# Kernel optimization log

Measured on AMD Instinct MI355X. Metric: run time of the kernel, lower is better.

Reference implementation:

```python
import jax, jax.numpy as jnp
import numpy as np

HEADS = 8

def _rotate_every_two(t):
    # t: [..., d]; interleaved rotation (-x2, x1) pairs
    x1 = t[..., ::2]
    x2 = t[..., 1::2]
    return jnp.stack([-x2, x1], axis=-1).reshape(t.shape)

def _theta_shift(t, sin, cos):
    return t * cos + _rotate_every_two(t) * sin

def setup_inputs() -> dict:
    key = jax.random.key(0)
    ks = jax.random.split(key, 5)
    B, H, W, C = 4, 40, 40, 512
    dh = C // HEADS
    x = jax.random.normal(ks[0], (B, H, W, C), dtype=jnp.float32)
    sin = jax.random.normal(ks[1], (H, W, dh), dtype=jnp.float32)
    cos = jax.random.normal(ks[2], (H, W, dh), dtype=jnp.float32)
    # 1x1 conv weight [3C, C] (kernel dims squeezed) + bias
    w_qkv = jax.random.normal(ks[3], (3 * C, C), dtype=jnp.float32) * (C ** -0.5)
    b_qkv = jnp.zeros((3 * C,), dtype=jnp.float32)
    return {"x": x, "sin": sin, "cos": cos, "w_qkv": w_qkv, "b_qkv": b_qkv}

def reference(x, sin, cos, w_qkv, b_qkv):
    B, H, W, C = x.shape
    heads = HEADS
    dh = C // heads
    scale = dh ** -0.5
    # 1x1 conv == per-pixel linear projection
    qkv = jnp.einsum('bhwc,oc->bhwo', x, w_qkv) + b_qkv  # [B,H,W,3C]
    q, k, v = jnp.split(qkv, 3, axis=-1)

    def to_heads(t):
        # channel order is (heads, dim_head) per the torch rearrange
        return t.reshape(B, H, W, heads, dh).transpose(0, 3, 1, 2, 4)  # [B,heads,H,W,dh]

    q = _theta_shift(to_heads(q), sin, cos)
    k = _theta_shift(to_heads(k), sin, cos)
    # v is computed but unused downstream in the original module (bug preserved)

    N = H * W
    q = q.reshape(B, heads, N, dh)
    k = k.reshape(B, heads, N, dh)

    attn = jnp.einsum('bhnd,bhmd->bhnm', q, k) * scale  # [B,heads,N,N]
    p = jax.nn.softmax(attn, axis=-1)
    # NOTE: original code does matmul(logist, kfine_heads) — K, not V. Kept faithful.
    out = jnp.einsum('bhnm,bhmd->bhnd', p, k)  # [B,heads,N,dh]
    out = out.transpose(0, 2, 1, 3).reshape(B, H, W, C)
    return out
```

## Files before the change

### kernel.cpp

```cpp
#include <hip/hip_runtime.h>
#include <hip/hip_bf16.h>


typedef __hip_bfloat16 bf16;
typedef __attribute__((ext_vector_type(8))) short short8;
typedef __attribute__((ext_vector_type(4))) short bfx4;
typedef __attribute__((ext_vector_type(4))) float f32x4;

#define NSP 1600
#define CDIM 512
#define DH 64

__device__ __forceinline__ f32x4 mfma32(short8 a, short8 b, f32x4 c) {
  return __builtin_amdgcn_mfma_f32_16x16x32_bf16(a, b, c, 0, 0, 0);
}

#if __has_builtin(__builtin_amdgcn_mfma_f32_16x16x16bf16_1k)
__device__ __forceinline__ f32x4 mfma_k16(bfx4 a, bfx4 b, f32x4 c) {
  return __builtin_amdgcn_mfma_f32_16x16x16bf16_1k(a, b, c, 0, 0, 0);
}
#else
__device__ __forceinline__ f32x4 mfma_k16(bfx4 a, bfx4 b, f32x4 c) {
  short8 a8 = {a.x, a.y, a.z, a.w, 0, 0, 0, 0};
  short8 b8 = {b.x, b.y, b.z, b.w, 0, 0, 0, 0};
  return __builtin_amdgcn_mfma_f32_16x16x32_bf16(a8, b8, c, 0, 0, 0);
}
#endif

__device__ __forceinline__ short8 cvt8(float4 v0, float4 v1) {
  short8 r; bf16* p = (bf16*)&r;
  p[0] = __float2bfloat16(v0.x); p[1] = __float2bfloat16(v0.y);
  p[2] = __float2bfloat16(v0.z); p[3] = __float2bfloat16(v0.w);
  p[4] = __float2bfloat16(v1.x); p[5] = __float2bfloat16(v1.y);
  p[6] = __float2bfloat16(v1.z); p[7] = __float2bfloat16(v1.w);
  return r;
}

extern "C" __global__ __launch_bounds__(256)
void cvt_kernel(const float* __restrict__ x, const float* __restrict__ w,
                const float* __restrict__ sin_t, const float* __restrict__ cos_t,
                bf16* __restrict__ x_bf, bf16* __restrict__ w_bf,
                float* __restrict__ sinT, float* __restrict__ cosT)
{
  __shared__ float t_lds[64][68];
  const int bid = blockIdx.x, tid = threadIdx.x;
  if (bid < 1600) {
    const size_t i = (size_t)bid * 2048 + tid * 8;
    float4 v0 = *(const float4*)(x + i);
    float4 v1 = *(const float4*)(x + i + 4);
    *(short8*)(x_bf + i) = cvt8(v0, v1);
  } else if (bid < 1856) {
    const size_t i = (size_t)(bid - 1600) * 2048 + tid * 8;
    float4 v0 = *(const float4*)(w + i);
    float4 v1 = *(const float4*)(w + i + 4);
    *(short8*)(w_bf + i) = cvt8(v0, v1);
  } else {
    const int t = bid - 1856;
    const float* src = (t < 25) ? sin_t : cos_t;
    float* dst = (t < 25) ? sinT : cosT;
    const int nt = (t < 25) ? t : t - 25;
    const int r = tid >> 2, c = (tid & 3) * 16;
#pragma unroll
    for (int j = 0; j < 4; ++j)
      *(float4*)&t_lds[r][c + j * 4] =
          *(const float4*)(src + (size_t)(nt * 64 + r) * 64 + c + j * 4);
    __syncthreads();
#pragma unroll
    for (int j4 = 0; j4 < 4; ++j4) {
      float4 o;
      o.x = t_lds[c + j4 * 4 + 0][r];
      o.y = t_lds[c + j4 * 4 + 1][r];
      o.z = t_lds[c + j4 * 4 + 2][r];
      o.w = t_lds[c + j4 * 4 + 3][r];
      *(float4*)(dst + (size_t)r * NSP + nt * 64 + c + j4 * 4) = o;
    }
  }
}

extern "C" __global__ __launch_bounds__(256)
void proj_kernel(const bf16* __restrict__ x_bf, const bf16* __restrict__ w_bf,
                 const float* __restrict__ bias, const float* __restrict__ sinT,
                 const float* __restrict__ cosT, bf16* __restrict__ q_ws,
                 bf16* __restrict__ k2_ws, bf16* __restrict__ kt2_ws)
{
  __shared__ __align__(16) char smem[27648];
  bf16 (*x_lds)[72] = (bf16(*)[72])smem;
  bf16 (*w_lds)[72] = (bf16(*)[72])(smem + 18432);
  bf16* ep = (bf16*)smem;

  const int tid  = threadIdx.x;
  const int wave = tid >> 6;
  const int lane = tid & 63;
  const int col  = lane & 15;
  const int quad = lane >> 4;
  const int wm = wave >> 1, wo = wave & 1;
  const int m0 = blockIdx.x * 128;
  const int o0 = blockIdx.y * 64;

  f32x4 acc[4][2];
#pragma unroll
  for (int i = 0; i < 4; ++i)
#pragma unroll
    for (int j = 0; j < 2; ++j) acc[i][j] = {0.f, 0.f, 0.f, 0.f};

  const int srow = tid >> 1;
  const int sch  = (tid & 1) * 32;
  const int wrow = tid >> 2;
  const int wch  = (tid & 3) * 16;

  for (int kt = 0; kt < 8; ++kt) {
    __syncthreads();
    {
      const bf16* xs = x_bf + (size_t)(m0 + srow) * CDIM + kt * 64 + sch;
#pragma unroll
      for (int j = 0; j < 4; ++j)
        *(short8*)&x_lds[srow][sch + j * 8] = *(const short8*)(xs + j * 8);
      const bf16* ws = w_bf + (size_t)(o0 + wrow) * CDIM + kt * 64 + wch;
#pragma unroll
      for (int j = 0; j < 2; ++j)
        *(short8*)&w_lds[wrow][wch + j * 8] = *(const short8*)(ws + j * 8);
    }
    __syncthreads();
#pragma unroll
    for (int half = 0; half < 2; ++half) {
      short8 af[4], bfr[2];
#pragma unroll
      for (int mt = 0; mt < 4; ++mt)
        af[mt] = *(short8*)&x_lds[wm * 64 + mt * 16 + col][half * 32 + quad * 8];
#pragma unroll
      for (int ot = 0; ot < 2; ++ot)
        bfr[ot] = *(short8*)&w_lds[wo * 32 + ot * 16 + col][half * 32 + quad * 8];
#pragma unroll
      for (int mt = 0; mt < 4; ++mt)
#pragma unroll
        for (int ot = 0; ot < 2; ++ot)
          acc[mt][ot] = mfma32(af[mt], bfr[ot], acc[mt][ot]);
    }
  }

  __syncthreads();
  const int b_idx = (m0 + wm * 64) / NSP;
  const int n0w   = m0 + wm * 64 - b_idx * NSP;
  const bool isq  = (o0 < 512);
#pragma unroll
  for (int ot = 0; ot < 2; ++ot) {
    const int o_local = wo * 32 + ot * 16 + col;
    const int o_g = o0 + o_local;
    const float bv = bias[o_g];
    const int d = o_g & 63;
#pragma unroll
    for (int mt = 0; mt < 4; ++mt) {
      const int nl = mt * 16 + quad * 4;
      float t[4], rot[4];
#pragma unroll
      for (int r = 0; r < 4; ++r) t[r] = acc[mt][ot][r] + bv;
#pragma unroll
      for (int r = 0; r < 4; ++r) {
        float tp = __shfl_xor(t[r], 1, 64);
        rot[r] = (lane & 1) ? tp : -tp;
      }
      const float4 c4 = *(const float4*)(cosT + (size_t)d * NSP + n0w + nl);
      const float4 s4 = *(const float4*)(sinT + (size_t)d * NSP + n0w + nl);
      float res[4];
      res[0] = t[0] * c4.x + rot[0] * s4.x;
      res[1] = t[1] * c4.y + rot[1] * s4.y;
      res[2] = t[2] * c4.z + rot[2] * s4.z;
      res[3] = t[3] * c4.w + rot[3] * s4.w;
      if (isq) {
#pragma unroll
        for (int r = 0; r < 4; ++r) res[r] *= 0.125f;
      }
      bfx4 pk; bf16* pp = (bf16*)&pk;
#pragma unroll
      for (int r = 0; r < 4; ++r) pp[r] = __float2bfloat16(res[r]);
      *(bfx4*)&ep[o_local * 132 + wm * 64 + nl] = pk;
    }
  }
  __syncthreads();

  if (isq) {
    const int m_l = tid >> 1, hf = tid & 1;
    const int gm = m0 + m_l;
    const int bi = gm / NSP, n = gm - bi * NSP;
    const int h = o0 >> 6;
    bf16* base = q_ws + ((size_t)(bi * 8 + h) * NSP + n) * 64 + hf * 32;
#pragma unroll
    for (int c = 0; c < 4; ++c) {
      short8 v; bf16* vp = (bf16*)&v;
#pragma unroll
      for (int j = 0; j < 8; ++j) vp[j] = ep[(hf * 32 + c * 8 + j) * 132 + m_l];
      *(short8*)(base + c * 8) = v;
    }
  } else {
    const int h = (o0 - 512) >> 6;
#pragma unroll
    for (int it = 0; it < 4; ++it) {
      const int ci = it * 256 + tid;
      const int T = (ci >> 9) & 1, inner = ci & 511;
      const int ccol = inner & 15, cq = (inner >> 4) & 3;
      const int f = (inner >> 6) & 1, ti = (inner >> 7) & 1, kh2 = (inner >> 8) & 1;
      const int gmb = m0 + T * 64;
      const int bi = gmb / NSP, ktile = (gmb - bi * NSP) >> 6;
      const int m_l = T * 64 + (2 * kh2 + ti) * 16 + ccol;
      const int er0 = (f * 4 + cq) * 8;
      short8 v; bf16* vp = (bf16*)&v;
#pragma unroll
      for (int j = 0; j < 8; ++j) vp[j] = ep[(er0 + j) * 132 + m_l];
      *(short8*)(k2_ws +
          (((size_t)(bi * 8 + h) * 25 + ktile) * 512 + inner) * 8) = v;
    }
#pragma unroll
    for (int it = 0; it < 4; ++it) {
      const int ci = it * 256 + tid;
      const int T = (ci >> 9) & 1, inner = ci & 511;
      const int ccol = inner & 15, cq = (inner >> 4) & 3;
      const int dt = (inner >> 6) & 3, kh2 = (inner >> 8) & 1;
      const int gmb = m0 + T * 64;
      const int bi = gmb / NSP, ktile = (gmb - bi * NSP) >> 6;
      const bf16* eprow =
          ep + (dt * 16 + ccol) * 132 + T * 64 + kh2 * 32 + cq * 4;
      short8 v;
      ((bfx4*)&v)[0] = *(const bfx4*)(eprow);
      ((bfx4*)&v)[1] = *(const bfx4*)(eprow + 16);
      *(short8*)(kt2_ws +
          (((size_t)(bi * 8 + h) * 25 + ktile) * 512 + inner) * 8) = v;
    }
  }
}


#define LOADF(KF, KTF, KT)                                                    \
  {                                                                           \
    const bf16* kc_  = k2b  + (KT) * 4096;                                    \
    const bf16* kc2_ = kt2b + (KT) * 4096;                                    \
    _Pragma("unroll")                                                         \
    for (int ti = 0; ti < 2; ++ti)                                            \
      _Pragma("unroll")                                                       \
      for (int f = 0; f < 2; ++f)                                             \
        KF[ti][f] =                                                           \
            *(const short8*)(kc_ + (((kh * 2 + ti) * 2 + f) * 64 + lane) * 8);\
    _Pragma("unroll")                                                         \
    for (int dt = 0; dt < 4; ++dt)                                            \
      KTF[dt] = *(const short8*)(kc2_ + ((kh * 4 + dt) * 64 + lane) * 8);     \
  }

#define COMPUTEF(KF, KTF)                                                     \
  {                                                                           \
    f32x4 s[2][2];                                                            \
    _Pragma("unroll")                                                         \
    for (int ti = 0; ti < 2; ++ti)                                            \
      _Pragma("unroll")                                                       \
      for (int ct = 0; ct < 2; ++ct) {                                        \
        f32x4 t = {0.f, 0.f, 0.f, 0.f};                                       \
        t = mfma32(KF[ti][0], qb[ct][0], t);                                  \
        t = mfma32(KF[ti][1], qb[ct][1], t);                                  \
        s[ti][ct] = t;                                                        \
      }                                                                       \
    bfx4 p4[2][2];                                                            \
    _Pragma("unroll")                                                         \
    for (int ti = 0; ti < 2; ++ti)                                            \
      _Pragma("unroll")                                                       \
      for (int ct = 0; ct < 2; ++ct) {                                        \
        _Pragma("unroll")                                                     \
        for (int r = 0; r < 4; ++r) s[ti][ct][r] = __expf(s[ti][ct][r]);      \
        l_part[ct] +=                                                         \
            s[ti][ct][0] + s[ti][ct][1] + s[ti][ct][2] + s[ti][ct][3];        \
        bf16* pp = (bf16*)&p4[ti][ct];                                        \
        _Pragma("unroll")                                                     \
        for (int r = 0; r < 4; ++r) pp[r] = __float2bfloat16(s[ti][ct][r]);   \
      }                                                                       \
    _Pragma("unroll")                                                         \
    for (int dt = 0; dt < 4; ++dt) {                                          \
      bfx4 alo = __builtin_shufflevector(KTF[dt], KTF[dt], 0, 1, 2, 3);       \
      bfx4 ahi = __builtin_shufflevector(KTF[dt], KTF[dt], 4, 5, 6, 7);       \
      _Pragma("unroll")                                                       \
      for (int ct = 0; ct < 2; ++ct) {                                        \
        oacc[dt][ct] = mfma_k16(alo, p4[0][ct], oacc[dt][ct]);                \
        oacc[dt][ct] = mfma_k16(ahi, p4[1][ct], oacc[dt][ct]);                \
      }                                                                       \
    }                                                                         \
  }

extern "C" __global__ __launch_bounds__(256, 2)
void attn_kernel(const bf16* __restrict__ q_ws, const bf16* __restrict__ k2_ws,
                 const bf16* __restrict__ kt2_ws, float* __restrict__ out)
{
  __shared__ float red[2][64][36];

  const int id = blockIdx.x;
  const int xr = id & 7, inner = id >> 3;
  const int qt = inner % 25;
  const int bh = (inner / 25) * 8 + xr;
  const int b = bh >> 3, h = bh & 7;
  const int tid  = threadIdx.x;
  const int wave = tid >> 6;
  const int lane = tid & 63;
  const int col  = lane & 15;
  const int quad = lane >> 4;
  const int qg = wave & 1, kh = wave >> 1;

  short8 qb[2][2];
#pragma unroll
  for (int ct = 0; ct < 2; ++ct) {
    const bf16* qp =
        q_ws + ((size_t)bh * NSP + qt * 64 + (qg * 2 + ct) * 16 + col) * 64;
    qb[ct][0] = *(const short8*)(qp + quad * 8);
    qb[ct][1] = *(const short8*)(qp + 32 + quad * 8);
  }

  f32x4 oacc[4][2];
#pragma unroll
  for (int i = 0; i < 4; ++i)
#pragma unroll
    for (int j = 0; j < 2; ++j) oacc[i][j] = {0.f, 0.f, 0.f, 0.f};
  float l_part[2] = {0.f, 0.f};

  const bf16* k2b  = k2_ws  + (size_t)bh * 25 * 4096;
  const bf16* kt2b = kt2_ws + (size_t)bh * 25 * 4096;

  short8 kfA[2][2], ktfA[4], kfB[2][2], ktfB[4];
  LOADF(kfA, ktfA, 0)
#pragma unroll 1
  for (int i = 0; i < 12; ++i) {
    LOADF(kfB, ktfB, 2 * i + 1)
    COMPUTEF(kfA, ktfA)
    LOADF(kfA, ktfA, 2 * i + 2)
    COMPUTEF(kfB, ktfB)
  }
  COMPUTEF(kfA, ktfA)

#pragma unroll
  for (int ct = 0; ct < 2; ++ct) {
    l_part[ct] += __shfl_xor(l_part[ct], 16, 64);
    l_part[ct] += __shfl_xor(l_part[ct], 32, 64);
  }

  if (wave >= 2) {
    float* dst = &red[wave - 2][lane][0];
#pragma unroll
    for (int dt = 0; dt < 4; ++dt)
#pragma unroll
      for (int ct = 0; ct < 2; ++ct)
        *(f32x4*)(dst + (dt * 2 + ct) * 4) = oacc[dt][ct];
    dst[32] = l_part[0]; dst[33] = l_part[1];
  }
  __syncthreads();
  if (wave < 2) {
    const float* srcr = &red[wave][lane][0];
#pragma unroll
    for (int dt = 0; dt < 4; ++dt)
#pragma unroll
      for (int ct = 0; ct < 2; ++ct)
        oacc[dt][ct] += *(const f32x4*)(srcr + (dt * 2 + ct) * 4);
    const float inv0 = 1.f / (l_part[0] + srcr[32]);
    const float inv1 = 1.f / (l_part[1] + srcr[33]);
#pragma unroll
    for (int ct = 0; ct < 2; ++ct) {
      const float inv = ct ? inv1 : inv0;
      const int qrow = qt * 64 + (qg * 2 + ct) * 16 + col;
      float* ob = out + ((size_t)b * NSP + qrow) * CDIM + h * 64;
#pragma unroll
      for (int dt = 0; dt < 4; ++dt) {
        float4 v;
        v.x = oacc[dt][ct][0] * inv; v.y = oacc[dt][ct][1] * inv;
        v.z = oacc[dt][ct][2] * inv; v.w = oacc[dt][ct][3] * inv;
        *(float4*)(ob + dt * 16 + quad * 4) = v;
      }
    }
  }
}

extern "C" void kernel_launch(void* const* d_in, const int* in_sizes, int n_in,
                              void* d_out, int out_size, void* d_ws, size_t ws_size,
                              hipStream_t stream) {
  const float* x     = (const float*)d_in[0];
  const float* sin_t = (const float*)d_in[1];
  const float* cos_t = (const float*)d_in[2];
  const float* w_qkv = (const float*)d_in[3];
  const float* b_qkv = (const float*)d_in[4];
  float* out = (float*)d_out;

  const size_t QK = (size_t)32 * NSP * DH;
  bf16* q_ws   = (bf16*)d_ws;
  bf16* k2_ws  = q_ws + QK;
  bf16* kt2_ws = k2_ws + QK;
  bf16* x_bf   = kt2_ws + QK;
  bf16* w_bf   = x_bf + (size_t)6400 * CDIM;
  float* sinT  = (float*)(w_bf + (size_t)1024 * CDIM);
  float* cosT  = sinT + (size_t)DH * NSP;

  cvt_kernel<<<1906, 256, 0, stream>>>(x, w_qkv, sin_t, cos_t, x_bf, w_bf, sinT, cosT);

  dim3 gproj(50, 16);
  proj_kernel<<<gproj, 256, 0, stream>>>(x_bf, w_bf, b_qkv, sinT, cosT,
                                         q_ws, k2_ws, kt2_ws);

  attn_kernel<<<800, 256, 0, stream>>>(q_ws, k2_ws, kt2_ws, out);
}
```

Measured before the change: 137.0 us.

## Split attention key tiles across eight waves per block with two-stage reduction

Doubles the attention block from 4 to 8 waves. Each wave now handles one 16-key subtile instead of two, so per-wave MFMA work, register fragments and the KT loads (now 4-element halves) are halved. The partial outputs and softmax denominators are combined with an extra LDS reduction stage and barrier. This aims to raise latency hiding and occupancy on the key loop, at the cost of more shared memory, more reduction traffic and an extra synchronization.

```diff
diff --git a/kernel.cpp b/kernel.cpp
--- a/kernel.cpp
+++ b/kernel.cpp
@@ -233,59 +233,46 @@
   {                                                                           \
     const bf16* kc_  = k2b  + (KT) * 4096;                                    \
     const bf16* kc2_ = kt2b + (KT) * 4096;                                    \
-    _Pragma("unroll")                                                         \
-    for (int ti = 0; ti < 2; ++ti)                                            \
-      _Pragma("unroll")                                                       \
-      for (int f = 0; f < 2; ++f)                                             \
-        KF[ti][f] =                                                           \
-            *(const short8*)(kc_ + (((kh * 2 + ti) * 2 + f) * 64 + lane) * 8);\
+    KF[0] = *(const short8*)(kc_ + ((kh * 2 + 0) * 64 + lane) * 8);           \
+    KF[1] = *(const short8*)(kc_ + ((kh * 2 + 1) * 64 + lane) * 8);           \
     _Pragma("unroll")                                                         \
     for (int dt = 0; dt < 4; ++dt)                                            \
-      KTF[dt] = *(const short8*)(kc2_ + ((kh * 4 + dt) * 64 + lane) * 8);     \
+      KTF[dt] =                                                               \
+          *(const bfx4*)(kc2_ + ((khh * 4 + dt) * 64 + lane) * 8 + khl * 4);  \
   }
 
 #define COMPUTEF(KF, KTF)                                                     \
   {                                                                           \
-    f32x4 s[2][2];                                                            \
+    f32x4 s[2];                                                               \
     _Pragma("unroll")                                                         \
-    for (int ti = 0; ti < 2; ++ti)                                            \
+    for (int ct = 0; ct < 2; ++ct) {                                          \
+      f32x4 t = {0.f, 0.f, 0.f, 0.f};                                         \
+      t = mfma32(KF[0], qb[ct][0], t);                                        \
+      t = mfma32(KF[1], qb[ct][1], t);                                        \
+      s[ct] = t;                                                              \
+    }                                                                         \
+    bfx4 p4[2];                                                               \
+    _Pragma("unroll")                                                         \
+    for (int ct = 0; ct < 2; ++ct) {                                          \
       _Pragma("unroll")                                                       \
-      for (int ct = 0; ct < 2; ++ct) {                                        \
-        f32x4 t = {0.f, 0.f, 0.f, 0.f};                                       \
-        t = mfma32(KF[ti][0], qb[ct][0], t);                                  \
-        t = mfma32(KF[ti][1], qb[ct][1], t);                                  \
-        s[ti][ct] = t;                                                        \
-      }                                                                       \
-    bfx4 p4[2][2];                                                            \
+      for (int r = 0; r < 4; ++r) s[ct][r] = __expf(s[ct][r]);                \
+      l_part[ct] += s[ct][0] + s[ct][1] + s[ct][2] + s[ct][3];                \
+      bf16* pp = (bf16*)&p4[ct];                                              \
+      _Pragma("unroll")                                                       \
+      for (int r = 0; r < 4; ++r) pp[r] = __float2bfloat16(s[ct][r]);         \
+    }                                                                         \
     _Pragma("unroll")                                                         \
-    for (int ti = 0; ti < 2; ++ti)                                            \
+    for (int dt = 0; dt < 4; ++dt)                                            \
       _Pragma("unroll")                                                       \
-      for (int ct = 0; ct < 2; ++ct) {                                        \
-        _Pragma("unroll")                                                     \
-        for (int r = 0; r < 4; ++r) s[ti][ct][r] = __expf(s[ti][ct][r]);      \
-        l_part[ct] +=                                                         \
-            s[ti][ct][0] + s[ti][ct][1] + s[ti][ct][2] + s[ti][ct][3];        \
-        bf16* pp = (bf16*)&p4[ti][ct];                                        \
-        _Pragma("unroll")                                                     \
-        for (int r = 0; r < 4; ++r) pp[r] = __float2bfloat16(s[ti][ct][r]);   \
-      }                                                                       \
-    _Pragma("unroll")                                                         \
-    for (int dt = 0; dt < 4; ++dt) {                                          \
-      bfx4 alo = __builtin_shufflevector(KTF[dt], KTF[dt], 0, 1, 2, 3);       \
-      bfx4 ahi = __builtin_shufflevector(KTF[dt], KTF[dt], 4, 5, 6, 7);       \
-      _Pragma("unroll")                                                       \
-      for (int ct = 0; ct < 2; ++ct) {                                        \
-        oacc[dt][ct] = mfma_k16(alo, p4[0][ct], oacc[dt][ct]);                \
-        oacc[dt][ct] = mfma_k16(ahi, p4[1][ct], oacc[dt][ct]);                \
-      }                                                                       \
-    }                                                                         \
-  }
-
-extern "C" __global__ __launch_bounds__(256, 2)
+      for (int ct = 0; ct < 2; ++ct)                                          \
+        oacc[dt][ct] = mfma_k16(KTF[dt], p4[ct], oacc[dt][ct]);               \
+  }
+
+extern "C" __global__ __launch_bounds__(512, 2)
 void attn_kernel(const bf16* __restrict__ q_ws, const bf16* __restrict__ k2_ws,
                  const bf16* __restrict__ kt2_ws, float* __restrict__ out)
 {
-  __shared__ float red[2][64][36];
+  __shared__ float red[4][64][36];
 
   const int id = blockIdx.x;
   const int xr = id & 7, inner = id >> 3;
@@ -297,7 +284,9 @@
   const int lane = tid & 63;
   const int col  = lane & 15;
   const int quad = lane >> 4;
-  const int qg = wave & 1, kh = wave >> 1;
+  const int qg = wave & 1;
+  const int kh = wave >> 1;
+  const int khh = kh >> 1, khl = kh & 1;
 
   short8 qb[2][2];
 #pragma unroll
@@ -318,7 +307,8 @@
   const bf16* k2b  = k2_ws  + (size_t)bh * 25 * 4096;
   const bf16* kt2b = kt2_ws + (size_t)bh * 25 * 4096;
 
-  short8 kfA[2][2], ktfA[4], kfB[2][2], ktfB[4];
+  short8 kfA[2], kfB[2];
+  bfx4 ktfA[4], ktfB[4];
   LOADF(kfA, ktfA, 0)
 #pragma unroll 1
   for (int i = 0; i < 12; ++i) {
@@ -335,7 +325,27 @@
     l_part[ct] += __shfl_xor(l_part[ct], 32, 64);
   }
 
-  if (wave >= 2) {
+  if (wave >= 4) {
+    float* dst = &red[wave - 4][lane][0];
+#pragma unroll
+    for (int dt = 0; dt < 4; ++dt)
+#pragma unroll
+      for (int ct = 0; ct < 2; ++ct)
+        *(f32x4*)(dst + (dt * 2 + ct) * 4) = oacc[dt][ct];
+    dst[32] = l_part[0]; dst[33] = l_part[1];
+  }
+  __syncthreads();
+  if (wave < 4) {
+    const float* srcr = &red[wave][lane][0];
+#pragma unroll
+    for (int dt = 0; dt < 4; ++dt)
+#pragma unroll
+      for (int ct = 0; ct < 2; ++ct)
+        oacc[dt][ct] += *(const f32x4*)(srcr + (dt * 2 + ct) * 4);
+    l_part[0] += srcr[32]; l_part[1] += srcr[33];
+  }
+  __syncthreads();
+  if (wave == 2 || wave == 3) {
     float* dst = &red[wave - 2][lane][0];
 #pragma unroll
     for (int dt = 0; dt < 4; ++dt)
@@ -395,5 +405,5 @@
   proj_kernel<<<gproj, 256, 0, stream>>>(x_bf, w_bf, b_qkv, sinT, cosT,
                                          q_ws, k2_ws, kt2_ws);
 
-  attn_kernel<<<800, 256, 0, stream>>>(q_ws, k2_ws, kt2_ws, out);
-}
+  attn_kernel<<<800, 512, 0, stream>>>(q_ws, k2_ws, kt2_ws, out);
+}
```

After: 145.5 us. 6.2% more time.
